# Performance work log

Measured on AMD Instinct MI355X. Metric: run time of the kernel, lower is better.

## Reference

```python
import jax, jax.numpy as jnp
import numpy as np

TRAN_DIM = 768
N_HEADS = 8
HEAD_DIM = 96
INNER = N_HEADS * HEAD_DIM  # 768


def setup_inputs() -> dict:
    key = jax.random.key(0)
    k1, k2, k3, k4, k5 = jax.random.split(key, 5)
    x = jax.random.normal(k1, (16, 1024, TRAN_DIM), dtype=jnp.float32)
    s_in = 1.0 / np.sqrt(TRAN_DIM)
    W_qkv = jax.random.uniform(k2, (TRAN_DIM, INNER * 3), jnp.float32, -s_in, s_in)
    b_qkv = jax.random.uniform(k3, (INNER * 3,), jnp.float32, -s_in, s_in)
    s_o = 1.0 / np.sqrt(INNER)
    W_out = jax.random.uniform(k4, (INNER, TRAN_DIM), jnp.float32, -s_o, s_o)
    b_out = jax.random.uniform(k5, (TRAN_DIM,), jnp.float32, -s_o, s_o)
    return {"x": x, "W_qkv": W_qkv, "b_qkv": b_qkv, "W_out": W_out, "b_out": b_out}


def reference(x, W_qkv, b_qkv, W_out, b_out):
    B, N, _ = x.shape
    qkv = x @ W_qkv + b_qkv  # [B, N, 3*INNER]
    q, k, v = jnp.split(qkv, 3, axis=-1)
    # [B, N, INNER] -> [B, H, N, D]
    def to_heads(t):
        return t.reshape(B, N, N_HEADS, HEAD_DIM).transpose(0, 2, 1, 3)
    q, k, v = to_heads(q), to_heads(k), to_heads(v)
    scale = HEAD_DIM ** (-0.5)
    dots = jnp.einsum('bhnd,bhmd->bhnm', q, k) * scale
    attn = jax.nn.softmax(dots, axis=-1)
    out = jnp.einsum('bhnm,bhmd->bhnd', attn, v)
    out = out.transpose(0, 2, 1, 3).reshape(B, N, INNER)
    return out @ W_out + b_out
```

## Files before the change

kernel.cpp:

```cpp
#include <hip/hip_runtime.h>
#include <hip/hip_bf16.h>


#define DEVINL __device__ __forceinline__

typedef __attribute__((ext_vector_type(8))) short s16x8;
typedef __attribute__((ext_vector_type(4))) short s16x4;
typedef __attribute__((ext_vector_type(4))) float f32x4;
typedef __attribute__((ext_vector_type(16))) float f32x16;

DEVINL short f2bf(float f) {
  union { float f; unsigned u; } c; c.f = f;
  unsigned r = c.u + 0x7FFFu + ((c.u >> 16) & 1u);
  return (short)(r >> 16);
}
DEVINL float asf(unsigned u) {
  union { unsigned u; float f; } c; c.u = u; return c.f;
}
DEVINL unsigned pack2(float a, float b) {
  union { float f; unsigned u; } ca, cb; ca.f = a; cb.f = b;
  return (ca.u >> 16) | (cb.u & 0xffff0000u);
}
DEVINL int swap23(int k) { return (k & ~12) | ((k & 4) << 1) | ((k & 8) >> 1); }

DEVINL void gload_lds16(const short* g, short* lds) {
  __builtin_amdgcn_global_load_lds((const __attribute__((address_space(1))) void*)g,
                                   (__attribute__((address_space(3))) void*)lds, 16, 0, 0);
}


__global__ void cvt_x_kernel(const float* __restrict__ in, short* __restrict__ out) {
  int i = blockIdx.x * 256 + threadIdx.x;
  float4 v = ((const float4*)in)[i];
  s16x4 o = { f2bf(v.x), f2bf(v.y), f2bf(v.z), f2bf(v.w) };
  *(s16x4*)(out + (size_t)i * 4) = o;
}

__global__ void tcvt_kernel(const float* __restrict__ in, short* __restrict__ out, int R, int C) {
  __shared__ float t[32][33];
  int tx = threadIdx.x & 31, ty = threadIdx.x >> 5;
  int r0 = blockIdx.y * 32, c0 = blockIdx.x * 32;
#pragma unroll
  for (int i = 0; i < 4; i++) {
    int r = ty + i * 8;
    t[r][tx] = in[(size_t)(r0 + r) * C + c0 + tx];
  }
  __syncthreads();
#pragma unroll
  for (int i = 0; i < 4; i++) {
    int r = ty + i * 8;
    out[(size_t)(c0 + r) * R + r0 + tx] = f2bf(t[tx][r]);
  }
}


template <int MODE>
__global__ __launch_bounds__(512, 4) void gemm2(const short* __restrict__ A, const short* __restrict__ Bt,
                                                const float* __restrict__ bias, int K, int nTn,
                                                short* __restrict__ qkvb, short* __restrict__ vtb,
                                                float* __restrict__ outf) {
  __shared__ short lds[36864];
  short* const ldsA = lds;
  short* const ldsB = lds + 24576;
  const int tid = threadIdx.x;
  const int l = tid & 63, w = tid >> 6;
  const int lo = l & 15, hi = l >> 4;
  const int wm = w >> 1, wn = w & 1;

  int cpx = gridDim.x >> 3;
  int bid = blockIdx.x;
  int swz = (bid & 7) * cpx + (bid >> 3);
  int tm = swz / nTn, tn = swz - tm * nTn;

  const int NKT = K >> 5;

  const int Ls = tid >> 3, s7 = tid & 7;
  const int pS = (s7 >> 2) & 1;
  const int cS = (s7 & 3) ^ (Ls & 3);
  const int rho = 2 * Ls + pS;
  const int gA = ((rho >> 5) << 6) + (rho & 31);
  const short* aS0 = A + (size_t)(tm * 256 + gA) * K + cS * 8;
  const short* aS1 = aS0 + (size_t)32 * K;
  const short* bS = Bt + (size_t)(tn * 128 + rho) * K + cS * 8;

#define ST_A(j, q, bs) gload_lds16(((q) ? aS1 : aS0) + (j) * 32, ldsA + ((bs) * 2 + (q)) * 4096 + tid * 8)
#define ST_B(j, bs)    gload_lds16(bS + (j) * 32, ldsB + (bs) * 4096 + tid * 8)

  const int LaBase = wm * 16 + (lo >> 1);
  const int LbBase = wn * 32 + (lo >> 1);
  const int pp = (lo & 1) << 2;

  f32x4 acc[4][4] = {};

#define RD_A(AF, bc, qm) do {                                                    \
    const short* base_ = ldsA + ((bc) * 2 + (qm)) * 4096;                        \
    _Pragma("unroll") for (int mi = 0; mi < 2; mi++) {                           \
      int La_ = LaBase + mi * 8;                                                 \
      AF[mi] = *(const s16x8*)(base_ + La_ * 64 + (((hi ^ (La_ & 3)) + pp) << 3)); } } while (0)
#define RD_B(BF, bc) do {                                                        \
    const short* base_ = ldsB + (bc) * 4096;                                     \
    _Pragma("unroll") for (int b = 0; b < 4; b++) {                              \
      int Lb_ = LbBase + b * 8;                                                  \
      BF[b] = *(const s16x8*)(base_ + Lb_ * 64 + (((hi ^ (Lb_ & 3)) + pp) << 3)); } } while (0)

#define MM8(a0, AF, BF) do {                                                     \
    __builtin_amdgcn_s_setprio(1);                                               \
    _Pragma("unroll") for (int mi = 0; mi < 2; mi++)                             \
      _Pragma("unroll") for (int b = 0; b < 4; b++)                              \
        acc[(a0) + mi][b] = __builtin_amdgcn_mfma_f32_16x16x32_bf16(             \
            AF[mi], BF[b], acc[(a0) + mi][b], 0, 0, 0);                          \
    __builtin_amdgcn_s_setprio(0); } while (0)

#define WAITV(n) asm volatile("s_waitcnt vmcnt(" #n ")" ::: "memory")
#define BARR() do { __builtin_amdgcn_sched_barrier(0); __builtin_amdgcn_s_barrier(); \
                    __builtin_amdgcn_sched_barrier(0); } while (0)

  ST_A(0, 0, 0); ST_B(0, 0); ST_A(0, 1, 0);
  ST_A(1, 0, 1); ST_B(1, 1); ST_A(1, 1, 1);
  WAITV(3);
  __builtin_amdgcn_s_barrier();

  s16x8 af[2], bf[4];
  int bc = 0;
#pragma unroll 1
  for (int kt = 0; kt < NKT; kt++) {
    int bs = (bc == 0) ? 2 : bc - 1;
    RD_A(af, bc, 0);
    RD_B(bf, bc);
    if (kt + 2 < NKT) { ST_A(kt + 2, 0, bs); ST_B(kt + 2, bs); }
    MM8(0, af, bf);
    RD_A(af, bc, 1);
    if (kt + 2 < NKT) ST_A(kt + 2, 1, bs);
    MM8(2, af, bf);
    if (kt + 2 < NKT) {
      WAITV(3);
    } else if (kt + 2 == NKT) {
      WAITV(0);
    }
    BARR();
    bc = (bc == 2) ? 0 : bc + 1;
  }
#undef ST_A
#undef ST_B
#undef RD_A
#undef RD_B
#undef MM8
#undef WAITV
#undef BARR

  if (MODE == 0) {
    const float qscale = 0.14724444757204526f;
    __syncthreads();
    if (tn < 12) {
#pragma unroll
      for (int b = 0; b < 4; b++) {
        int colr = wn * 64 + b * 16 + lo;
        int coln = tn * 128 + colr;
        float bv = bias[coln];
        float scl = (coln < 768) ? qscale : 1.0f;
#pragma unroll
        for (int a = 0; a < 4; a++)
#pragma unroll
          for (int j = 0; j < 4; j++) {
            int rowr = wm * 64 + a * 16 + hi * 4 + j;
            lds[rowr * 128 + colr] = f2bf((acc[a][b][j] + bv) * scl);
          }
      }
      __syncthreads();
      short* dstb = qkvb + (size_t)(tm * 256) * 2304 + tn * 128;
#pragma unroll
      for (int k = 0; k < 8; k++) {
        int g = k * 512 + tid;
        int r = g >> 4, c = g & 15;
        *(s16x8*)(dstb + (size_t)r * 2304 + c * 8) = *(const s16x8*)(lds + r * 128 + c * 8);
      }
    } else {
      short* scr = lds + w * 4096;
#pragma unroll
      for (int b = 0; b < 4; b++) {
        int c = b * 16 + lo;
        float bv = bias[tn * 128 + wn * 64 + c];
#pragma unroll
        for (int a = 0; a < 4; a++)
#pragma unroll
          for (int j = 0; j < 4; j++) {
            int row = a * 16 + hi * 4 + j;
            scr[row * 64 + (c ^ (((row >> 3) & 7) << 3))] = f2bf(acc[a][b][j] + bv);
          }
      }
      int r8 = l >> 3, k8 = l & 7;
      int n0 = k8 * 8;
      int rowg = tm * 256 + wm * 64;
      int bb = rowg >> 10;
      int nb = (rowg & 1023) + n0;
#pragma unroll
      for (int p = 0; p < 8; p++) {
        int c = p * 8 + r8;
        int inner = tn * 128 + wn * 64 + c - 1536;
        int hh = inner / 96;
        int dd = inner - hh * 96;
        union { short v[8]; s16x8 x; } t;
#pragma unroll
        for (int j = 0; j < 8; j++)
          t.v[j] = scr[(n0 + j) * 64 + (c ^ (k8 << 3))];
        *(s16x8*)(vtb + ((size_t)(bb * 8 + hh) * 96 + dd) * 1024 + nb) = t.x;
      }
    }
  } else {
#pragma unroll
    for (int b = 0; b < 4; b++) {
      int coln = tn * 128 + wn * 64 + b * 16 + lo;
      float bv = bias[coln];
#pragma unroll
      for (int a = 0; a < 4; a++)
#pragma unroll
        for (int j = 0; j < 4; j++) {
          int rowm = tm * 256 + wm * 64 + a * 16 + hi * 4 + j;
          outf[(size_t)rowm * 768 + coln] = acc[a][b][j] + bv;
        }
    }
  }
}


__global__ __launch_bounds__(256) void attn_kernel(const short* __restrict__ qkvb,
                                                   const short* __restrict__ vtb,
                                                   short* __restrict__ attn_out) {
  __shared__ short Klds[2 * 64 * 104];
  __shared__ short Vlds[2 * 96 * 64];
  const int KOFF = 64 * 104, VOFF = 96 * 64;
  int tid = threadIdx.x, lane = tid & 63, wid = tid >> 6;
  int q31 = lane & 31, hi2 = lane >> 5;
  int bid = blockIdx.x;
  int pair = bid & 127, qt = bid >> 7;
  int b = pair >> 3, h = pair & 7;
  const short* Vtp = vtb + (size_t)pair * 1024 * 96;
  int qrow0 = qt * 128 + wid * 32;

  s16x8 qf[6];
#pragma unroll
  for (int dc = 0; dc < 6; dc++)
    qf[dc] = *(const s16x8*)(qkvb + (size_t)(b * 1024 + qrow0 + q31) * 2304 +
                             h * 96 + dc * 16 + hi2 * 8);

  const short* sp[6];
  short* sdst[6];
  int sstep[6], boff[6];
#pragma unroll
  for (int i = 0; i < 6; i++) {
    if (i < 3) {
      int c = i * 256 + tid;
      int krow = c / 12, kcc = c - krow * 12;
      int lam = swap23(krow);
      sdst[i] = Klds + lam * 104 + kcc * 8;
      sp[i] = qkvb + (size_t)(b * 1024 + krow) * 2304 + 768 + h * 96 + kcc * 8;
      sstep[i] = 64 * 2304;
      boff[i] = KOFF;
    } else {
      int d = (i - 3) * 256 + tid;
      int vrow = d >> 3, vcc = d & 7;
      sdst[i] = Vlds + vrow * 64 + ((vcc ^ (vrow & 7)) << 3);
      sp[i] = Vtp + (size_t)vrow * 1024 + vcc * 8;
      sstep[i] = 64;
      boff[i] = VOFF;
    }
  }

  f32x16 accO[3] = {};
  float lsum = 0.0f;

  s16x8 sreg[6];
#pragma unroll
  for (int i = 0; i < 6; i++) sreg[i] = *(const s16x8*)sp[i];
#pragma unroll
  for (int i = 0; i < 6; i++) *(s16x8*)sdst[i] = sreg[i];
#pragma unroll
  for (int i = 0; i < 6; i++) sreg[i] = *(const s16x8*)(sp[i] + (size_t)sstep[i]);
  __syncthreads();

  for (int t = 0; t < 16; t++) {
    int cur = t & 1, nxt = (t + 1) & 1;
    if (t < 15) {
#pragma unroll
      for (int i = 0; i < 6; i++) *(s16x8*)(sdst[i] + nxt * boff[i]) = sreg[i];
      int t2 = (t + 2) & 15;
#pragma unroll
      for (int i = 0; i < 6; i++)
        sreg[i] = *(const s16x8*)(sp[i] + (size_t)t2 * sstep[i]);
    }

    const short* Kb = Klds + cur * KOFF;
    const short* Vb = Vlds + cur * VOFF;
#pragma unroll
    for (int kb = 0; kb < 2; kb++) {
      f32x16 st = {};
      __builtin_amdgcn_s_setprio(1);
#pragma unroll
      for (int dc = 0; dc < 6; dc++) {
        int c = dc * 2 + hi2;
        int lam = kb * 32 + q31;
        s16x8 kf = *(const s16x8*)(Kb + lam * 104 + c * 8);
        st = __builtin_amdgcn_mfma_f32_32x32x16_bf16(kf, qf[dc], st, 0, 0, 0);
      }
      __builtin_amdgcn_s_setprio(0);

      unsigned u[8];
#pragma unroll
      for (int i = 0; i < 8; i++) {
        float p0 = __builtin_amdgcn_exp2f(st[2 * i]);
        float p1 = __builtin_amdgcn_exp2f(st[2 * i + 1]);
        unsigned w = pack2(p0, p1);
        u[i] = w;
        lsum += asf(w << 16) + asf(w & 0xffff0000u);
      }

      __builtin_amdgcn_s_setprio(1);
#pragma unroll
      for (int half = 0; half < 2; half++) {
        union { unsigned w[4]; s16x8 v; } pa;
#pragma unroll
        for (int wi = 0; wi < 4; wi++) pa.w[wi] = u[half * 4 + wi];
        int kc = kb * 2 + half;
#pragma unroll
        for (int db = 0; db < 3; db++) {
          int d = db * 32 + q31;
          s16x8 vf = *(const s16x8*)(Vb + d * 64 + (((kc * 2 + hi2) ^ (d & 7)) << 3));
          accO[db] = __builtin_amdgcn_mfma_f32_32x32x16_bf16(pa.v, vf, accO[db], 0, 0, 0);
        }
      }
      __builtin_amdgcn_s_setprio(0);
    }
    __syncthreads();
  }

  float s = lsum + __shfl_xor(lsum, 32, 64);
  float rinv = 1.0f / s;
  float rr[16];
#pragma unroll
  for (int r = 0; r < 16; r++)
    rr[r] = __shfl(rinv, (r & 3) + 8 * (r >> 2) + 4 * hi2, 64);

#pragma unroll
  for (int db = 0; db < 3; db++)
#pragma unroll
    for (int r = 0; r < 16; r++) {
      int qrow = qrow0 + (r & 3) + 8 * (r >> 2) + 4 * hi2;
      int d = db * 32 + q31;
      attn_out[((size_t)b * 1024 + qrow) * 768 + h * 96 + d] = f2bf(accO[db][r] * rr[r]);
    }
}


extern "C" void kernel_launch(void* const* d_in, const int* in_sizes, int n_in,
                              void* d_out, int out_size, void* d_ws, size_t ws_size,
                              hipStream_t stream) {
  const float* x = (const float*)d_in[0];
  const float* Wqkv = (const float*)d_in[1];
  const float* bqkv = (const float*)d_in[2];
  const float* Wout = (const float*)d_in[3];
  const float* bout = (const float*)d_in[4];
  float* out = (float*)d_out;

  char* ws = (char*)d_ws;
  short* xb = (short*)ws;
  short* wqkvT = (short*)(ws + 25165824);
  short* woutT = (short*)(ws + 28704768);
  short* qkvb = (short*)(ws + 29884416);
  short* vtb = (short*)(ws + 105381888);

  cvt_x_kernel<<<12288, 256, 0, stream>>>(x, xb);
  tcvt_kernel<<<dim3(72, 24), 256, 0, stream>>>(Wqkv, wqkvT, 768, 2304);
  tcvt_kernel<<<dim3(24, 24), 256, 0, stream>>>(Wout, woutT, 768, 768);

  gemm2<0><<<1152, 512, 0, stream>>>(xb, wqkvT, bqkv, 768, 18, qkvb, vtb, nullptr);
  attn_kernel<<<1024, 256, 0, stream>>>(qkvb, vtb, xb);
  gemm2<1><<<384, 512, 0, stream>>>(xb, woutT, bout, 768, 6, nullptr, nullptr, out);
}
```

Baseline: 182.6 us.

## Fuse fp32-to-bf16 conversion of x into the QKV GEMM A-tile loads

Removes the separate conversion kernel for x and instead has the QKV GEMM load fp32 rows into registers, convert them with packed bf16 instructions, and store them to LDS. The B operand still uses direct global-to-LDS loads. This is meant to save a full read/write pass over x and one kernel launch. In exchange, the A operand traffic doubles in size and now flows through registers with extra waits in the pipelined loop.

```diff
diff --git a/kernel.cpp b/kernel.cpp
--- a/kernel.cpp
+++ b/kernel.cpp
@@ -29,13 +29,6 @@
 }
 
 
-__global__ void cvt_x_kernel(const float* __restrict__ in, short* __restrict__ out) {
-  int i = blockIdx.x * 256 + threadIdx.x;
-  float4 v = ((const float4*)in)[i];
-  s16x4 o = { f2bf(v.x), f2bf(v.y), f2bf(v.z), f2bf(v.w) };
-  *(s16x4*)(out + (size_t)i * 4) = o;
-}
-
 __global__ void tcvt_kernel(const float* __restrict__ in, short* __restrict__ out, int R, int C) {
   __shared__ float t[32][33];
   int tx = threadIdx.x & 31, ty = threadIdx.x >> 5;
@@ -54,10 +47,188 @@
 }
 
 
-template <int MODE>
+__global__ __launch_bounds__(512, 4) void gemm2f(const float* __restrict__ Ax, const short* __restrict__ Bt,
+                                                 const float* __restrict__ bias, int nTn,
+                                                 short* __restrict__ qkvb, short* __restrict__ vtb) {
+  __shared__ short lds[36864];
+  short* const ldsA = lds;
+  short* const ldsB = lds + 24576;
+  const int tid = threadIdx.x;
+  const int l = tid & 63, w = tid >> 6;
+  const int lo = l & 15, hi = l >> 4;
+  const int wm = w >> 1, wn = w & 1;
+
+  int cpx = gridDim.x >> 3;
+  int bid = blockIdx.x;
+  int swz = (bid & 7) * cpx + (bid >> 3);
+  int tm = swz / nTn, tn = swz - tm * nTn;
+
+  const int NKT = 24;
+
+  const int Ls = tid >> 3, s7 = tid & 7;
+  const int pS = (s7 >> 2) & 1;
+  const int cS = (s7 & 3) ^ (Ls & 3);
+  const int rho = 2 * Ls + pS;
+  const int gA = ((rho >> 5) << 6) + (rho & 31);
+  const float* aF = Ax + (size_t)(tm * 256 + gA) * 768 + cS * 8;
+  const short* bS = Bt + (size_t)(tn * 128 + rho) * 768 + cS * 8;
+  short* const bD = ldsB + tid * 8;
+
+  float4 ar0, ar1, ar2, ar3;
+
+#define L_A(j) do {                                                   \
+    const float* p_ = aF + (j) * 32;                                  \
+    ar0 = *(const float4*)p_;                                         \
+    ar1 = *(const float4*)(p_ + 4);                                   \
+    ar2 = *(const float4*)(p_ + 32 * 768);                            \
+    ar3 = *(const float4*)(p_ + 32 * 768 + 4); } while (0)
+
+#define CVTPK(d, a, b) asm("v_cvt_pk_bf16_f32 %0, %1, %2" : "=v"(d) : "v"(a), "v"(b))
+
+#define CW_A(bs) do {                                                 \
+    union { unsigned w4[4]; s16x8 v; } t0_, t1_;                      \
+    CVTPK(t0_.w4[0], ar0.x, ar0.y); CVTPK(t0_.w4[1], ar0.z, ar0.w);   \
+    CVTPK(t0_.w4[2], ar1.x, ar1.y); CVTPK(t0_.w4[3], ar1.z, ar1.w);   \
+    CVTPK(t1_.w4[0], ar2.x, ar2.y); CVTPK(t1_.w4[1], ar2.z, ar2.w);   \
+    CVTPK(t1_.w4[2], ar3.x, ar3.y); CVTPK(t1_.w4[3], ar3.z, ar3.w);   \
+    *(s16x8*)(ldsA + ((bs) * 2 + 0) * 4096 + tid * 8) = t0_.v;        \
+    *(s16x8*)(ldsA + ((bs) * 2 + 1) * 4096 + tid * 8) = t1_.v; } while (0)
+
+#define ST_B(j, bs) gload_lds16(bS + (j) * 32, bD + (bs) * 4096)
+
+  const int LaBase = wm * 16 + (lo >> 1);
+  const int LbBase = wn * 32 + (lo >> 1);
+  const int pp = (lo & 1) << 2;
+
+  f32x4 acc[4][4] = {};
+
+#define RD_A(AF, bc, qm) do {                                                    \
+    const short* base_ = ldsA + ((bc) * 2 + (qm)) * 4096;                        \
+    _Pragma("unroll") for (int mi = 0; mi < 2; mi++) {                           \
+      int La_ = LaBase + mi * 8;                                                 \
+      AF[mi] = *(const s16x8*)(base_ + La_ * 64 + (((hi ^ (La_ & 3)) + pp) << 3)); } } while (0)
+#define RD_B(BF, bc) do {                                                        \
+    const short* base_ = ldsB + (bc) * 4096;                                     \
+    _Pragma("unroll") for (int b = 0; b < 4; b++) {                              \
+      int Lb_ = LbBase + b * 8;                                                  \
+      BF[b] = *(const s16x8*)(base_ + Lb_ * 64 + (((hi ^ (Lb_ & 3)) + pp) << 3)); } } while (0)
+
+#define MM8(a0, AF, BF) do {                                                     \
+    __builtin_amdgcn_s_setprio(1);                                               \
+    _Pragma("unroll") for (int mi = 0; mi < 2; mi++)                             \
+      _Pragma("unroll") for (int b = 0; b < 4; b++)                              \
+        acc[(a0) + mi][b] = __builtin_amdgcn_mfma_f32_16x16x32_bf16(             \
+            AF[mi], BF[b], acc[(a0) + mi][b], 0, 0, 0);                          \
+    __builtin_amdgcn_s_setprio(0); } while (0)
+
+#define WAITV(n) asm volatile("s_waitcnt vmcnt(" #n ")" ::: "memory")
+#define WAITL() asm volatile("s_waitcnt lgkmcnt(0)" ::: "memory")
+#define BARR() do { __builtin_amdgcn_sched_barrier(0); __builtin_amdgcn_s_barrier(); \
+                    __builtin_amdgcn_sched_barrier(0); } while (0)
+
+  L_A(0);
+  ST_B(0, 0); ST_B(1, 1);
+  WAITV(1);
+  CW_A(0);
+  WAITL();
+  __builtin_amdgcn_s_barrier();
+
+  s16x8 af[2], bf[4];
+  int bc = 0;
+#pragma unroll 1
+  for (int kt = 0; kt < NKT; kt++) {
+    int bn = (bc == 2) ? 0 : bc + 1;
+    int bs = (bc == 0) ? 2 : bc - 1;
+    if (kt + 1 < NKT) L_A(kt + 1);
+    if (kt + 2 < NKT) ST_B(kt + 2, bs);
+    RD_A(af, bc, 0);
+    RD_B(bf, bc);
+    MM8(0, af, bf);
+    RD_A(af, bc, 1);
+    MM8(2, af, bf);
+    if (kt + 1 < NKT) {
+      if (kt + 2 < NKT) { WAITV(1); } else { WAITV(0); }
+      CW_A(bn);
+      WAITL();
+    }
+    BARR();
+    bc = bn;
+  }
+#undef L_A
+#undef CVTPK
+#undef CW_A
+#undef ST_B
+#undef RD_A
+#undef RD_B
+#undef MM8
+#undef WAITV
+#undef WAITL
+#undef BARR
+
+  {
+    const float qscale = 0.14724444757204526f;
+    __syncthreads();
+    if (tn < 12) {
+#pragma unroll
+      for (int b = 0; b < 4; b++) {
+        int colr = wn * 64 + b * 16 + lo;
+        int coln = tn * 128 + colr;
+        float bv = bias[coln];
+        float scl = (coln < 768) ? qscale : 1.0f;
+#pragma unroll
+        for (int a = 0; a < 4; a++)
+#pragma unroll
+          for (int j = 0; j < 4; j++) {
+            int rowr = wm * 64 + a * 16 + hi * 4 + j;
+            lds[rowr * 128 + colr] = f2bf((acc[a][b][j] + bv) * scl);
+          }
+      }
+      __syncthreads();
+      short* dstb = qkvb + (size_t)(tm * 256) * 2304 + tn * 128;
+#pragma unroll
+      for (int k = 0; k < 8; k++) {
+        int g = k * 512 + tid;
+        int r = g >> 4, c = g & 15;
+        *(s16x8*)(dstb + (size_t)r * 2304 + c * 8) = *(const s16x8*)(lds + r * 128 + c * 8);
+      }
+    } else {
+      short* scr = lds + w * 4096;
+#pragma unroll
+      for (int b = 0; b < 4; b++) {
+        int c = b * 16 + lo;
+        float bv = bias[tn * 128 + wn * 64 + c];
+#pragma unroll
+        for (int a = 0; a < 4; a++)
+#pragma unroll
+          for (int j = 0; j < 4; j++) {
+            int row = a * 16 + hi * 4 + j;
+            scr[row * 64 + (c ^ (((row >> 3) & 7) << 3))] = f2bf(acc[a][b][j] + bv);
+          }
+      }
+      int r8 = l >> 3, k8 = l & 7;
+      int n0 = k8 * 8;
+      int rowg = tm * 256 + wm * 64;
+      int bb = rowg >> 10;
+      int nb = (rowg & 1023) + n0;
+#pragma unroll
+      for (int p = 0; p < 8; p++) {
+        int c = p * 8 + r8;
+        int inner = tn * 128 + wn * 64 + c - 1536;
+        int hh = inner / 96;
+        int dd = inner - hh * 96;
+        union { short v[8]; s16x8 x; } t;
+#pragma unroll
+        for (int j = 0; j < 8; j++)
+          t.v[j] = scr[(n0 + j) * 64 + (c ^ (k8 << 3))];
+        *(s16x8*)(vtb + ((size_t)(bb * 8 + hh) * 96 + dd) * 1024 + nb) = t.x;
+      }
+    }
+  }
+}
+
+
 __global__ __launch_bounds__(512, 4) void gemm2(const short* __restrict__ A, const short* __restrict__ Bt,
                                                 const float* __restrict__ bias, int K, int nTn,
-                                                short* __restrict__ qkvb, short* __restrict__ vtb,
                                                 float* __restrict__ outf) {
   __shared__ short lds[36864];
   short* const ldsA = lds;
@@ -148,77 +319,17 @@
 #undef WAITV
 #undef BARR
 
-  if (MODE == 0) {
-    const float qscale = 0.14724444757204526f;
-    __syncthreads();
-    if (tn < 12) {
-#pragma unroll
-      for (int b = 0; b < 4; b++) {
-        int colr = wn * 64 + b * 16 + lo;
-        int coln = tn * 128 + colr;
-        float bv = bias[coln];
-        float scl = (coln < 768) ? qscale : 1.0f;
-#pragma unroll
-        for (int a = 0; a < 4; a++)
-#pragma unroll
-          for (int j = 0; j < 4; j++) {
-            int rowr = wm * 64 + a * 16 + hi * 4 + j;
-            lds[rowr * 128 + colr] = f2bf((acc[a][b][j] + bv) * scl);
-          }
-      }
-      __syncthreads();
-      short* dstb = qkvb + (size_t)(tm * 256) * 2304 + tn * 128;
-#pragma unroll
-      for (int k = 0; k < 8; k++) {
-        int g = k * 512 + tid;
-        int r = g >> 4, c = g & 15;
-        *(s16x8*)(dstb + (size_t)r * 2304 + c * 8) = *(const s16x8*)(lds + r * 128 + c * 8);
-      }
-    } else {
-      short* scr = lds + w * 4096;
-#pragma unroll
-      for (int b = 0; b < 4; b++) {
-        int c = b * 16 + lo;
-        float bv = bias[tn * 128 + wn * 64 + c];
-#pragma unroll
-        for (int a = 0; a < 4; a++)
-#pragma unroll
-          for (int j = 0; j < 4; j++) {
-            int row = a * 16 + hi * 4 + j;
-            scr[row * 64 + (c ^ (((row >> 3) & 7) << 3))] = f2bf(acc[a][b][j] + bv);
-          }
-      }
-      int r8 = l >> 3, k8 = l & 7;
-      int n0 = k8 * 8;
-      int rowg = tm * 256 + wm * 64;
-      int bb = rowg >> 10;
-      int nb = (rowg & 1023) + n0;
-#pragma unroll
-      for (int p = 0; p < 8; p++) {
-        int c = p * 8 + r8;
-        int inner = tn * 128 + wn * 64 + c - 1536;
-        int hh = inner / 96;
-        int dd = inner - hh * 96;
-        union { short v[8]; s16x8 x; } t;
-#pragma unroll
-        for (int j = 0; j < 8; j++)
-          t.v[j] = scr[(n0 + j) * 64 + (c ^ (k8 << 3))];
-        *(s16x8*)(vtb + ((size_t)(bb * 8 + hh) * 96 + dd) * 1024 + nb) = t.x;
-      }
-    }
-  } else {
-#pragma unroll
-    for (int b = 0; b < 4; b++) {
-      int coln = tn * 128 + wn * 64 + b * 16 + lo;
-      float bv = bias[coln];
-#pragma unroll
-      for (int a = 0; a < 4; a++)
-#pragma unroll
-        for (int j = 0; j < 4; j++) {
-          int rowm = tm * 256 + wm * 64 + a * 16 + hi * 4 + j;
-          outf[(size_t)rowm * 768 + coln] = acc[a][b][j] + bv;
-        }
-    }
+#pragma unroll
+  for (int b = 0; b < 4; b++) {
+    int coln = tn * 128 + wn * 64 + b * 16 + lo;
+    float bv = bias[coln];
+#pragma unroll
+    for (int a = 0; a < 4; a++)
+#pragma unroll
+      for (int j = 0; j < 4; j++) {
+        int rowm = tm * 256 + wm * 64 + a * 16 + hi * 4 + j;
+        outf[(size_t)rowm * 768 + coln] = acc[a][b][j] + bv;
+      }
   }
 }
 
@@ -368,11 +479,10 @@
   short* qkvb = (short*)(ws + 29884416);
   short* vtb = (short*)(ws + 105381888);
 
-  cvt_x_kernel<<<12288, 256, 0, stream>>>(x, xb);
   tcvt_kernel<<<dim3(72, 24), 256, 0, stream>>>(Wqkv, wqkvT, 768, 2304);
   tcvt_kernel<<<dim3(24, 24), 256, 0, stream>>>(Wout, woutT, 768, 768);
 
-  gemm2<0><<<1152, 512, 0, stream>>>(xb, wqkvT, bqkv, 768, 18, qkvb, vtb, nullptr);
+  gemm2f<<<1152, 512, 0, stream>>>(x, wqkvT, bqkv, 18, qkvb, vtb);
   attn_kernel<<<1024, 256, 0, stream>>>(qkvb, vtb, xb);
-  gemm2<1><<<384, 512, 0, stream>>>(xb, woutT, bout, 768, 6, nullptr, nullptr, out);
-}
+  gemm2<<<384, 512, 0, stream>>>(xb, woutT, bout, 768, 6, out);
+}
```

Measured after the change: 186.2 us. About the same (+2.0%).
